# Performance work log

Hardware: AMD Instinct MI355X
Metric: run time of the kernel (lower is better)

The kernel has to match this reference:

```python
import jax, jax.numpy as jnp
import numpy as np

B, S, D, H, DH = 2, 2048, 1024, 16, 64
LN_EPS = 1e-5

def _layernorm(x, g, b):
    mu = jnp.mean(x, axis=-1, keepdims=True)
    var = jnp.mean(jnp.square(x - mu), axis=-1, keepdims=True)
    return (x - mu) * jax.lax.rsqrt(var + LN_EPS) * g + b

def setup_inputs() -> dict:
    key = jax.random.key(0)
    ks = jax.random.split(key, 12)
    s = 0.02
    return {
        'x': jax.random.normal(ks[0], (B, S, D), jnp.float32),
        'attention_mask': jnp.zeros((B, S), jnp.bool_),
        'Wq': jax.random.normal(ks[1], (H, D, DH), jnp.float32) * s,
        'bq': jnp.zeros((H, DH), jnp.float32),
        'Wk': jax.random.normal(ks[2], (H, D, DH), jnp.float32) * s,
        'bk': jnp.zeros((H, DH), jnp.float32),
        'Wv': jax.random.normal(ks[3], (H, D, DH), jnp.float32) * s,
        'bv': jnp.zeros((H, DH), jnp.float32),
        'ln_g': jnp.ones((D,), jnp.float32),
        'ln_b': jnp.zeros((D,), jnp.float32),
        'W1': jax.random.normal(ks[4], (D, 4 * D), jnp.float32) * s,
        'b1': jnp.zeros((4 * D,), jnp.float32),
        'W2': jax.random.normal(ks[5], (4 * D, D), jnp.float32) * s,
        'b2': jnp.zeros((D,), jnp.float32),
    }

def reference(x, attention_mask, Wq, bq, Wk, bk, Wv, bv, ln_g, ln_b, W1, b1, W2, b2):
    # NOTE: source has a typo bug ('attentoin_score'), so the attention_mask is
    # computed-then-discarded; softmax is applied to the UNMASKED scaled scores.
    dh = Wq.shape[-1]
    q = jnp.einsum('bsd,hde->bhse', x, Wq) + bq[:, None, :]  # [B,H,S,dh]
    k = jnp.einsum('bsd,hde->bhse', x, Wk) + bk[:, None, :]
    v = jnp.einsum('bsd,hde->bhse', x, Wv) + bv[:, None, :]
    scores = jnp.einsum('bhse,bhte->bhst', q, k) / jnp.sqrt(jnp.float32(dh))
    attn = jax.nn.softmax(scores, axis=-1)
    o = jnp.einsum('bhst,bhte->bhse', attn, v)  # [B,H,S,dh]
    b_, h_, s_, e_ = o.shape
    # concat heads along last dim == transpose then reshape
    mha = jnp.transpose(o, (0, 2, 1, 3)).reshape(b_, s_, h_ * e_)
    h1 = _layernorm(x + mha, ln_g, ln_b)
    ffn = jax.nn.relu(h1 @ W1 + b1) @ W2 + b2
    return _layernorm(h1 + ffn, ln_g, ln_b)
```

## Files before the change

kernel.cpp:

```cpp
#include <hip/hip_runtime.h>

#define DEVI __device__ __forceinline__

typedef __attribute__((ext_vector_type(8))) __bf16 bf16x8;
typedef __attribute__((ext_vector_type(4))) float f32x4;
typedef __attribute__((ext_vector_type(4))) unsigned short u16x4;
typedef __attribute__((ext_vector_type(8))) unsigned short u16x8;

static DEVI unsigned short f2bf(float f) {
  unsigned int i = __float_as_uint(f);
  i += 0x7fffu + ((i >> 16) & 1u);
  return (unsigned short)(i >> 16);
}

static DEVI unsigned short f2bfh(float f) {
  union { __bf16 h; unsigned short u; } c;
  c.h = (__bf16)f;
  return c.u;
}

static DEVI float bf2f(unsigned short u) {
  return __uint_as_float((unsigned int)u << 16);
}

static DEVI f32x4 mfma16x16x32(bf16x8 a, bf16x8 b, f32x4 c) {
  return __builtin_amdgcn_mfma_f32_16x16x32_bf16(a, b, c, 0, 0, 0);
}

static DEVI void async_ld16(const void* g, void* lds) {
  __builtin_amdgcn_global_load_lds(
      (const __attribute__((address_space(1))) void*)g,
      (__attribute__((address_space(3))) void*)lds, 16, 0, 0);
}

template <int BN, int OUT_MODE, bool RELU>
static DEVI void gemm_bt_core(const unsigned short* __restrict__ A, int lda,
                              const unsigned short* __restrict__ Bt, int ldb,
                              int K, int m0, int n0,
                              const float* __restrict__ bias,
                              void* __restrict__ Cp, int ldc,
                              const float* __restrict__ bq,
                              const float* __restrict__ bk,
                              const float* __restrict__ bv,
                              unsigned short* __restrict__ qo,
                              unsigned short* __restrict__ ko,
                              unsigned short* __restrict__ vo) {
  constexpr int MT = (BN == 128) ? 4 : 2;
  constexpr int NT = 4;
  __shared__ __align__(16) unsigned short As[128 * 32];
  __shared__ __align__(16) unsigned short Bs[BN * 32];

  const int tid = threadIdx.x;
  const int w = tid >> 6, l = tid & 63;
  const int lr = l & 15, lq = l >> 4;
  const int wm0 = (BN == 128) ? ((w >> 1) * 64) : (w * 32);
  const int wn0 = (BN == 128) ? ((w & 1) * 64) : 0;
  const int lrow = l >> 2;
  const int lcol = (l & 3) * 8;

  f32x4 acc[MT][NT];
#pragma unroll
  for (int i = 0; i < MT; ++i)
#pragma unroll
    for (int j = 0; j < NT; ++j) acc[i][j] = (f32x4){0.f, 0.f, 0.f, 0.f};

  for (int kb = 0; kb < K; kb += 32) {
#pragma unroll
    for (int p = 0; p < 2; ++p) {
      const int r0 = p * 64 + w * 16;
      async_ld16(A + (size_t)(m0 + r0 + lrow) * lda + kb + lcol, As + r0 * 32);
    }
#pragma unroll
    for (int p = 0; p < BN / 64; ++p) {
      const int r0 = p * 64 + w * 16;
      async_ld16(Bt + (size_t)(n0 + r0 + lrow) * ldb + kb + lcol, Bs + r0 * 32);
    }
    __syncthreads();

    bf16x8 af[MT], bfr[NT];
#pragma unroll
    for (int mt = 0; mt < MT; ++mt)
      af[mt] = *(const bf16x8*)(As + (wm0 + mt * 16 + lr) * 32 + lq * 8);
#pragma unroll
    for (int nt = 0; nt < NT; ++nt)
      bfr[nt] = *(const bf16x8*)(Bs + (wn0 + nt * 16 + lr) * 32 + lq * 8);
#pragma unroll
    for (int mt = 0; mt < MT; ++mt)
#pragma unroll
      for (int nt = 0; nt < NT; ++nt)
        acc[mt][nt] = mfma16x16x32(af[mt], bfr[nt], acc[mt][nt]);
    __syncthreads();
  }

#pragma unroll
  for (int mt = 0; mt < MT; ++mt) {
    const int grow = m0 + wm0 + mt * 16 + lq * 4;
#pragma unroll
    for (int nt = 0; nt < NT; ++nt) {
      const int gcol = n0 + wn0 + nt * 16 + lr;
      if (OUT_MODE == 2) {
        const int which = gcol >> 10;
        const int h = (gcol >> 6) & 15;
        const int e = gcol & 63;
        const float* bp = (which == 0) ? bq : (which == 1) ? bk : bv;
        const float bvv = bp[gcol & 1023];
        unsigned short* op = (which == 0) ? qo : (which == 1) ? ko : vo;
#pragma unroll
        for (int r = 0; r < 4; ++r) {
          const int row = grow + r;
          const int b_ = row >> 11, s_ = row & 2047;
          const size_t base = (size_t)((b_ << 4) + h) * 131072 + (size_t)s_ * 64;
          if (which == 1) {
            const int o = e >> 3;
            const int pos = (((o ^ (s_ & 7)) << 3) | (e & 7));
            op[base + pos] = f2bf((acc[mt][nt][r] + bvv) * 0.18033688011112f);
          } else {
            op[base + e] = f2bf(acc[mt][nt][r] + bvv);
          }
        }
      } else if (OUT_MODE == 3) {
#pragma unroll
        for (int r = 0; r < 4; ++r)
          ((unsigned short*)Cp)[(size_t)(grow + r) * ldc + gcol] =
              f2bf(acc[mt][nt][r]);
      } else {
        const float bvv = bias[gcol];
#pragma unroll
        for (int r = 0; r < 4; ++r) {
          float val = acc[mt][nt][r] + bvv;
          if (RELU) val = fmaxf(val, 0.f);
          if (OUT_MODE == 1)
            ((unsigned short*)Cp)[(size_t)(grow + r) * ldc + gcol] = f2bf(val);
          else
            ((float*)Cp)[(size_t)(grow + r) * ldc + gcol] = val;
        }
      }
    }
  }
}

__global__ __launch_bounds__(256) void k_gemm_qkv(
    const unsigned short* __restrict__ xb, const unsigned short* __restrict__ Wt,
    const float* __restrict__ bq, const float* __restrict__ bk,
    const float* __restrict__ bv, unsigned short* __restrict__ qo,
    unsigned short* __restrict__ ko, unsigned short* __restrict__ vo) {
  gemm_bt_core<128, 2, false>(xb, 1024, Wt, 1024, 1024, blockIdx.x * 128,
                              blockIdx.y * 128, nullptr, nullptr, 0, bq, bk, bv,
                              qo, ko, vo);
}

__global__ __launch_bounds__(256) void k_ffn1(
    const unsigned short* __restrict__ h1b, const unsigned short* __restrict__ W1t,
    const float* __restrict__ b1, unsigned short* __restrict__ f1) {
  gemm_bt_core<128, 1, true>(h1b, 1024, W1t, 1024, 1024, blockIdx.x * 128,
                             blockIdx.y * 128, b1, f1, 4096, nullptr, nullptr,
                             nullptr, nullptr, nullptr, nullptr);
}

__global__ __launch_bounds__(256) void k_ffn2(
    const unsigned short* __restrict__ f1, const unsigned short* __restrict__ W2t,
    unsigned short* __restrict__ pbase) {
  const int z = blockIdx.z;
  unsigned short* p = pbase + (size_t)z * 4194304;
  gemm_bt_core<128, 3, false>(f1 + z * 1024, 4096, W2t + z * 1024, 4096, 1024,
                              blockIdx.x * 128, blockIdx.y * 128, nullptr, p,
                              1024, nullptr, nullptr, nullptr, nullptr, nullptr,
                              nullptr);
}

__global__ __launch_bounds__(256) void k_cvt(const float* __restrict__ src,
                                             unsigned short* __restrict__ dst) {
  const size_t i = ((size_t)blockIdx.x * 256 + threadIdx.x) * 4;
  f32x4 v = *(const f32x4*)(src + i);
  u16x4 pk;
#pragma unroll
  for (int j = 0; j < 4; ++j) pk[j] = f2bf(v[j]);
  *(u16x4*)(dst + i) = pk;
}

static DEVI void tr64(const float* __restrict__ s, int sld,
                      unsigned short* __restrict__ d, int dld) {
  __shared__ float t[64][65];
  const int tr = threadIdx.x >> 4;
  const int tc4 = (threadIdx.x & 15) * 4;
#pragma unroll
  for (int i = 0; i < 4; ++i) {
    f32x4 v = *(const f32x4*)(s + (size_t)(i * 16 + tr) * sld + tc4);
#pragma unroll
    for (int j = 0; j < 4; ++j) t[i * 16 + tr][tc4 + j] = v[j];
  }
  __syncthreads();
#pragma unroll
  for (int i = 0; i < 4; ++i) {
    const int c = i * 16 + tr;
    u16x4 pk;
#pragma unroll
    for (int j = 0; j < 4; ++j) pk[j] = f2bf(t[tc4 + j][c]);
    *(u16x4*)(d + (size_t)c * dld + tc4) = pk;
  }
}

__global__ __launch_bounds__(256) void k_twall(
    const float* __restrict__ Wq, const float* __restrict__ Wk,
    const float* __restrict__ Wv, const float* __restrict__ W1,
    const float* __restrict__ W2, unsigned short* __restrict__ wqkvt,
    unsigned short* __restrict__ w1t, unsigned short* __restrict__ w2t) {
  const int bid = blockIdx.x;
  if (bid < 768) {
    const int bx = bid & 15, by = bid >> 4;
    const int which = by >> 4, h = by & 15;
    const float* W = (which == 0) ? Wq : (which == 1) ? Wk : Wv;
    const float* s = W + (size_t)h * 65536;
    unsigned short* d = wqkvt + (size_t)(which * 1024 + h * 64) * 1024;
    const int r0 = bx * 64;
    tr64(s + (size_t)r0 * 64, 64, d + r0, 1024);
  } else if (bid < 1792) {
    const int t = bid - 768;
    const int bx = t & 15, by = t >> 4;
    const int r0 = bx * 64, c0 = by * 64;
    tr64(W1 + (size_t)r0 * 4096 + c0, 4096, w1t + (size_t)c0 * 1024 + r0, 1024);
  } else {
    const int t = bid - 1792;
    const int bx = t & 63, by = t >> 6;
    const int r0 = bx * 64, c0 = by * 64;
    tr64(W2 + (size_t)r0 * 1024 + c0, 1024, w2t + (size_t)c0 * 4096 + r0, 4096);
  }
}

__global__ __launch_bounds__(256) void k_vprep(const unsigned short* __restrict__ vb,
                                               unsigned short* __restrict__ vp) {
  const int bh = blockIdx.y, t = blockIdx.x;
  __shared__ unsigned short tl[64][72];
  const int tid = threadIdx.x;
  const size_t base = (size_t)bh * 131072;
  const int kr = tid >> 3, oc = tid & 7;
#pragma unroll
  for (int p = 0; p < 2; ++p) {
    const int key = p * 32 + kr;
    *(u16x8*)&tl[key][oc * 8] =
        *(const u16x8*)(vb + base + (size_t)(t * 64 + key) * 64 + oc * 8);
  }
  __syncthreads();
#pragma unroll
  for (int p = 0; p < 2; ++p) {
    const int dh = p * 32 + kr;
    const int ok = oc ^ (dh & 7);
    u16x8 pk;
#pragma unroll
    for (int j = 0; j < 8; ++j) {
      const int kap = ok * 8 + j;
      const int key = (kap & 3) * 16 + (kap >> 2);
      pk[j] = tl[key][dh];
    }
    *(u16x8*)(vp + base + (size_t)dh * 2048 + t * 64 + oc * 8) = pk;
  }
}

__global__ __launch_bounds__(512) void k_attn(
    const unsigned short* __restrict__ q, const unsigned short* __restrict__ ks,
    const unsigned short* __restrict__ vp, float* __restrict__ mha) {
  const int bid = blockIdx.x;
  const int bh = (bid & 7) * 4 + ((bid >> 3) >> 4);
  const int qt = (bid >> 3) & 15;
  const int b = bh >> 4, h = bh & 15;
  const int tid = threadIdx.x;
  const int w = tid >> 6, l = tid & 63;
  const int lr = l & 15, lq = l >> 4, l7 = lr & 7;

  __shared__ __align__(16) unsigned short Ks[2][64 * 64];
  __shared__ __align__(16) unsigned short Vt[2][64 * 64];
  __shared__ __align__(16) unsigned short Ps[8][16][72];

  const size_t bho = (size_t)bh * 131072;
  const int q0 = qt * 128 + w * 16;

  bf16x8 qf0, qf1;
  {
    const unsigned short* qp = q + bho + (size_t)(q0 + lr) * 64 + lq * 8;
    qf0 = *(const bf16x8*)qp;
    qf1 = *(const bf16x8*)(qp + 32);
  }

  f32x4 l_acc[4];
  f32x4 o[4];
#pragma unroll
  for (int i = 0; i < 4; ++i) {
    l_acc[i] = (f32x4){0.f, 0.f, 0.f, 0.f};
    o[i] = (f32x4){0.f, 0.f, 0.f, 0.f};
  }

  const unsigned short* kg = ks + bho;
  const unsigned short* vg = vp + bho;
  const int srow = l >> 3, scol = (l & 7) * 8;
  const int r0 = w * 8;

  async_ld16(kg + (size_t)(r0 + srow) * 64 + scol, &Ks[0][r0 * 64]);
  async_ld16(vg + (size_t)(r0 + srow) * 2048 + scol, &Vt[0][r0 * 64]);
  __syncthreads();

  for (int kt = 0; kt < 32; ++kt) {
    const int cur = kt & 1, nxt = cur ^ 1;
    if (kt + 1 < 32) {
      const int k1 = (kt + 1) * 64;
      async_ld16(kg + (size_t)(k1 + r0 + srow) * 64 + scol, &Ks[nxt][r0 * 64]);
      async_ld16(vg + (size_t)(r0 + srow) * 2048 + k1 + scol, &Vt[nxt][r0 * 64]);
    }

    bf16x8 kf[4][2];
#pragma unroll
    for (int ct = 0; ct < 4; ++ct)
#pragma unroll
      for (int hh = 0; hh < 2; ++hh)
        kf[ct][hh] = *(const bf16x8*)&Ks[cur][(ct * 16 + lr) * 64 +
                                             (((hh << 2) | lq) ^ l7) * 8];
    f32x4 s[4];
#pragma unroll
    for (int ct = 0; ct < 4; ++ct) {
      f32x4 t = {0.f, 0.f, 0.f, 0.f};
      t = mfma16x16x32(qf0, kf[ct][0], t);
      t = mfma16x16x32(qf1, kf[ct][1], t);
      s[ct] = t;
    }

#pragma unroll
    for (int r = 0; r < 4; ++r) {
      f32x4 pe;
#pragma unroll
      for (int ct = 0; ct < 4; ++ct)
        pe[ct] = __builtin_amdgcn_exp2f(s[ct][r]);
      l_acc[r] += pe;
      u16x4 pk;
#pragma unroll
      for (int ct = 0; ct < 4; ++ct) pk[ct] = f2bfh(pe[ct]);
      *(u16x4*)&Ps[w][lq * 4 + r][lr * 4] = pk;
    }
    __asm__ volatile("" ::: "memory");

    bf16x8 vf[4][2];
#pragma unroll
    for (int dt = 0; dt < 4; ++dt)
#pragma unroll
      for (int hh = 0; hh < 2; ++hh)
        vf[dt][hh] = *(const bf16x8*)&Vt[cur][(dt * 16 + lr) * 64 +
                                             (((hh << 2) | lq) ^ l7) * 8];
    bf16x8 pf0 = *(const bf16x8*)&Ps[w][lr][lq * 8];
    bf16x8 pf1 = *(const bf16x8*)&Ps[w][lr][32 + lq * 8];
#pragma unroll
    for (int dt = 0; dt < 4; ++dt) {
      o[dt] = mfma16x16x32(pf0, vf[dt][0], o[dt]);
      o[dt] = mfma16x16x32(pf1, vf[dt][1], o[dt]);
    }
    __syncthreads();
  }

#pragma unroll
  for (int r = 0; r < 4; ++r) {
    f32x4 la = l_acc[r];
    float sd = la[0] + la[1] + la[2] + la[3];
    sd += __shfl_xor(sd, 1);
    sd += __shfl_xor(sd, 2);
    sd += __shfl_xor(sd, 4);
    sd += __shfl_xor(sd, 8);
    const float inv = 1.f / sd;
    float* op = mha + ((size_t)b * 2048 + q0 + lq * 4 + r) * 1024 + h * 64 + lr;
    op[0] = o[0][r] * inv;
    op[16] = o[1][r] * inv;
    op[32] = o[2][r] * inv;
    op[48] = o[3][r] * inv;
  }
}

__global__ __launch_bounds__(256) void k_add_ln(const float* __restrict__ a,
                                                const float* __restrict__ b,
                                                const float* __restrict__ g,
                                                const float* __restrict__ be,
                                                unsigned short* __restrict__ outb) {
  const int row = blockIdx.x;
  const int tid = threadIdx.x;
  const size_t base = (size_t)row * 1024 + tid * 4;
  f32x4 va = *(const f32x4*)(a + base);
  f32x4 vb = *(const f32x4*)(b + base);
  f32x4 xx;
  float s = 0.f, q = 0.f;
#pragma unroll
  for (int i = 0; i < 4; ++i) {
    xx[i] = va[i] + vb[i];
    s += xx[i];
    q += xx[i] * xx[i];
  }
#pragma unroll
  for (int off = 1; off < 64; off <<= 1) {
    s += __shfl_xor(s, off);
    q += __shfl_xor(q, off);
  }
  __shared__ float ss[4], qs[4];
  const int w = tid >> 6;
  if ((tid & 63) == 0) { ss[w] = s; qs[w] = q; }
  __syncthreads();
  s = ss[0] + ss[1] + ss[2] + ss[3];
  q = qs[0] + qs[1] + qs[2] + qs[3];
  const float mean = s * (1.f / 1024.f);
  const float var = q * (1.f / 1024.f) - mean * mean;
  const float rstd = rsqrtf(var + 1e-5f);
  f32x4 vg = *(const f32x4*)(g + tid * 4);
  f32x4 vbe = *(const f32x4*)(be + tid * 4);
  u16x4 pk;
#pragma unroll
  for (int i = 0; i < 4; ++i)
    pk[i] = f2bf((xx[i] - mean) * rstd * vg[i] + vbe[i]);
  *(u16x4*)(outb + base) = pk;
}

__global__ __launch_bounds__(256) void k_add_ln4(
    const unsigned short* __restrict__ h1b, const unsigned short* __restrict__ pb,
    const float* __restrict__ cb, const float* __restrict__ g,
    const float* __restrict__ be, float* __restrict__ out) {
  const int row = blockIdx.x;
  const int tid = threadIdx.x;
  const size_t base = (size_t)row * 1024 + tid * 4;
  u16x4 uh = *(const u16x4*)(h1b + base);
  u16x4 up[4];
#pragma unroll
  for (int z = 0; z < 4; ++z)
    up[z] = *(const u16x4*)(pb + base + (size_t)z * 4194304);
  f32x4 vcb = *(const f32x4*)(cb + tid * 4);
  f32x4 xx;
  float s = 0.f, q = 0.f;
#pragma unroll
  for (int i = 0; i < 4; ++i) {
    float v = bf2f(uh[i]) + vcb[i];
#pragma unroll
    for (int z = 0; z < 4; ++z) v += bf2f(up[z][i]);
    xx[i] = v;
    s += v;
    q += v * v;
  }
#pragma unroll
  for (int off = 1; off < 64; off <<= 1) {
    s += __shfl_xor(s, off);
    q += __shfl_xor(q, off);
  }
  __shared__ float ss[4], qs[4];
  const int w = tid >> 6;
  if ((tid & 63) == 0) { ss[w] = s; qs[w] = q; }
  __syncthreads();
  s = ss[0] + ss[1] + ss[2] + ss[3];
  q = qs[0] + qs[1] + qs[2] + qs[3];
  const float mean = s * (1.f / 1024.f);
  const float var = q * (1.f / 1024.f) - mean * mean;
  const float rstd = rsqrtf(var + 1e-5f);
  f32x4 vg = *(const f32x4*)(g + tid * 4);
  f32x4 vbe = *(const f32x4*)(be + tid * 4);
  f32x4 ov;
#pragma unroll
  for (int i = 0; i < 4; ++i) ov[i] = (xx[i] - mean) * rstd * vg[i] + vbe[i];
  *(f32x4*)(out + base) = ov;
}

extern "C" void kernel_launch(void* const* d_in, const int* in_sizes, int n_in,
                              void* d_out, int out_size, void* d_ws,
                              size_t ws_size, hipStream_t stream) {
  const float* x = (const float*)d_in[0];
  const float* Wq = (const float*)d_in[2];
  const float* bq = (const float*)d_in[3];
  const float* Wk = (const float*)d_in[4];
  const float* bk = (const float*)d_in[5];
  const float* Wv = (const float*)d_in[6];
  const float* bv = (const float*)d_in[7];
  const float* lg = (const float*)d_in[8];
  const float* lb = (const float*)d_in[9];
  const float* W1 = (const float*)d_in[10];
  const float* b1 = (const float*)d_in[11];
  const float* W2 = (const float*)d_in[12];
  const float* b2 = (const float*)d_in[13];

  char* ws = (char*)d_ws;
  const size_t MB = 1024 * 1024;
  unsigned short* qb = (unsigned short*)(ws + 0);
  unsigned short* kb = (unsigned short*)(ws + 8 * MB);
  unsigned short* vb = (unsigned short*)(ws + 16 * MB);
  unsigned short* vp = (unsigned short*)(ws + 24 * MB);
  unsigned short* f1 = (unsigned short*)(ws + 0);
  unsigned short* xb = (unsigned short*)(ws + 32 * MB);
  unsigned short* pb = (unsigned short*)(ws + 32 * MB);
  float* mha = (float*)(ws + 40 * MB);
  unsigned short* h1b = (unsigned short*)(ws + 64 * MB);
  unsigned short* wqkvt = (unsigned short*)(ws + 72 * MB);
  unsigned short* w1t = (unsigned short*)(ws + 78 * MB);
  unsigned short* w2t = (unsigned short*)(ws + 86 * MB);

  k_cvt<<<dim3(4096), 256, 0, stream>>>(x, xb);
  k_twall<<<dim3(2816), 256, 0, stream>>>(Wq, Wk, Wv, W1, W2, wqkvt, w1t, w2t);

  k_gemm_qkv<<<dim3(32, 24), 256, 0, stream>>>(xb, wqkvt, bq, bk, bv, qb, kb, vb);
  k_vprep<<<dim3(32, 32), 256, 0, stream>>>(vb, vp);
  k_attn<<<dim3(512), 512, 0, stream>>>(qb, kb, vp, mha);
  k_add_ln<<<dim3(4096), 256, 0, stream>>>(x, mha, lg, lb, h1b);
  k_ffn1<<<dim3(32, 32), 256, 0, stream>>>(h1b, w1t, b1, f1);
  k_ffn2<<<dim3(32, 8, 4), 256, 0, stream>>>(f1, w2t, pb);
  k_add_ln4<<<dim3(4096), 256, 0, stream>>>(h1b, pb, b2, lg, lb, (float*)d_out);
}
```

Baseline: 324.0 us.

## Fuse V permutation into QKV GEMM epilogue, merge prep kernels, store attention output bf16

The QKV GEMM epilogue now writes V straight into the swizzled, transposed layout that attention consumes, so the separate k_vprep kernel and its intermediate buffer are gone. The x-to-bf16 conversion is folded into the weight-transpose kernel as one k_prep launch. The attention output is stored as bf16 instead of fp32, which halves that write and the read in the add+layernorm kernel. The cost is scattered 2-byte stores for V in the epilogue and reduced precision on the attention output before the residual add.

```diff
diff --git a/kernel.cpp b/kernel.cpp
--- a/kernel.cpp
+++ b/kernel.cpp
@@ -104,18 +104,23 @@
         const int e = gcol & 63;
         const float* bp = (which == 0) ? bq : (which == 1) ? bk : bv;
         const float bvv = bp[gcol & 1023];
-        unsigned short* op = (which == 0) ? qo : (which == 1) ? ko : vo;
 #pragma unroll
         for (int r = 0; r < 4; ++r) {
           const int row = grow + r;
           const int b_ = row >> 11, s_ = row & 2047;
-          const size_t base = (size_t)((b_ << 4) + h) * 131072 + (size_t)s_ * 64;
-          if (which == 1) {
+          const size_t base = (size_t)((b_ << 4) + h) * 131072;
+          const float val = acc[mt][nt][r] + bvv;
+          if (which == 0) {
+            qo[base + (size_t)s_ * 64 + e] = f2bf(val);
+          } else if (which == 1) {
             const int o = e >> 3;
             const int pos = (((o ^ (s_ & 7)) << 3) | (e & 7));
-            op[base + pos] = f2bf((acc[mt][nt][r] + bvv) * 0.18033688011112f);
+            ko[base + (size_t)s_ * 64 + pos] = f2bf(val * 0.18033688011112f);
           } else {
-            op[base + e] = f2bf(acc[mt][nt][r] + bvv);
+            const int t = s_ >> 6, k64 = s_ & 63;
+            const int kap = (k64 & 15) * 4 + (k64 >> 4);
+            const int pos = (((kap >> 3) ^ (e & 7)) << 3) | (kap & 7);
+            vo[base + (size_t)e * 2048 + t * 64 + pos] = f2bf(val);
           }
         }
       } else if (OUT_MODE == 3) {
@@ -168,16 +173,6 @@
                               nullptr);
 }
 
-__global__ __launch_bounds__(256) void k_cvt(const float* __restrict__ src,
-                                             unsigned short* __restrict__ dst) {
-  const size_t i = ((size_t)blockIdx.x * 256 + threadIdx.x) * 4;
-  f32x4 v = *(const f32x4*)(src + i);
-  u16x4 pk;
-#pragma unroll
-  for (int j = 0; j < 4; ++j) pk[j] = f2bf(v[j]);
-  *(u16x4*)(dst + i) = pk;
-}
-
 static DEVI void tr64(const float* __restrict__ s, int sld,
                       unsigned short* __restrict__ d, int dld) {
   __shared__ float t[64][65];
@@ -200,65 +195,48 @@
   }
 }
 
-__global__ __launch_bounds__(256) void k_twall(
-    const float* __restrict__ Wq, const float* __restrict__ Wk,
-    const float* __restrict__ Wv, const float* __restrict__ W1,
-    const float* __restrict__ W2, unsigned short* __restrict__ wqkvt,
+__global__ __launch_bounds__(256) void k_prep(
+    const float* __restrict__ x, const float* __restrict__ Wq,
+    const float* __restrict__ Wk, const float* __restrict__ Wv,
+    const float* __restrict__ W1, const float* __restrict__ W2,
+    unsigned short* __restrict__ xb, unsigned short* __restrict__ wqkvt,
     unsigned short* __restrict__ w1t, unsigned short* __restrict__ w2t) {
   const int bid = blockIdx.x;
-  if (bid < 768) {
-    const int bx = bid & 15, by = bid >> 4;
+  if (bid < 1024) {
+    const size_t i0 = ((size_t)bid * 256 + threadIdx.x) * 16;
+#pragma unroll
+    for (int c = 0; c < 4; ++c) {
+      f32x4 v = *(const f32x4*)(x + i0 + c * 4);
+      u16x4 pk;
+#pragma unroll
+      for (int j = 0; j < 4; ++j) pk[j] = f2bf(v[j]);
+      *(u16x4*)(xb + i0 + c * 4) = pk;
+    }
+  } else if (bid < 1792) {
+    const int t = bid - 1024;
+    const int bx = t & 15, by = t >> 4;
     const int which = by >> 4, h = by & 15;
     const float* W = (which == 0) ? Wq : (which == 1) ? Wk : Wv;
     const float* s = W + (size_t)h * 65536;
     unsigned short* d = wqkvt + (size_t)(which * 1024 + h * 64) * 1024;
     const int r0 = bx * 64;
     tr64(s + (size_t)r0 * 64, 64, d + r0, 1024);
-  } else if (bid < 1792) {
-    const int t = bid - 768;
+  } else if (bid < 2816) {
+    const int t = bid - 1792;
     const int bx = t & 15, by = t >> 4;
     const int r0 = bx * 64, c0 = by * 64;
     tr64(W1 + (size_t)r0 * 4096 + c0, 4096, w1t + (size_t)c0 * 1024 + r0, 1024);
   } else {
-    const int t = bid - 1792;
+    const int t = bid - 2816;
     const int bx = t & 63, by = t >> 6;
     const int r0 = bx * 64, c0 = by * 64;
     tr64(W2 + (size_t)r0 * 1024 + c0, 1024, w2t + (size_t)c0 * 4096 + r0, 4096);
   }
 }
 
-__global__ __launch_bounds__(256) void k_vprep(const unsigned short* __restrict__ vb,
-                                               unsigned short* __restrict__ vp) {
-  const int bh = blockIdx.y, t = blockIdx.x;
-  __shared__ unsigned short tl[64][72];
-  const int tid = threadIdx.x;
-  const size_t base = (size_t)bh * 131072;
-  const int kr = tid >> 3, oc = tid & 7;
-#pragma unroll
-  for (int p = 0; p < 2; ++p) {
-    const int key = p * 32 + kr;
-    *(u16x8*)&tl[key][oc * 8] =
-        *(const u16x8*)(vb + base + (size_t)(t * 64 + key) * 64 + oc * 8);
-  }
-  __syncthreads();
-#pragma unroll
-  for (int p = 0; p < 2; ++p) {
-    const int dh = p * 32 + kr;
-    const int ok = oc ^ (dh & 7);
-    u16x8 pk;
-#pragma unroll
-    for (int j = 0; j < 8; ++j) {
-      const int kap = ok * 8 + j;
-      const int key = (kap & 3) * 16 + (kap >> 2);
-      pk[j] = tl[key][dh];
-    }
-    *(u16x8*)(vp + base + (size_t)dh * 2048 + t * 64 + oc * 8) = pk;
-  }
-}
-
 __global__ __launch_bounds__(512) void k_attn(
     const unsigned short* __restrict__ q, const unsigned short* __restrict__ ks,
-    const unsigned short* __restrict__ vp, float* __restrict__ mha) {
+    const unsigned short* __restrict__ vp, unsigned short* __restrict__ mha) {
   const int bid = blockIdx.x;
   const int bh = (bid & 7) * 4 + ((bid >> 3) >> 4);
   const int qt = (bid >> 3) & 15;
@@ -362,16 +340,17 @@
     sd += __shfl_xor(sd, 4);
     sd += __shfl_xor(sd, 8);
     const float inv = 1.f / sd;
-    float* op = mha + ((size_t)b * 2048 + q0 + lq * 4 + r) * 1024 + h * 64 + lr;
-    op[0] = o[0][r] * inv;
-    op[16] = o[1][r] * inv;
-    op[32] = o[2][r] * inv;
-    op[48] = o[3][r] * inv;
+    unsigned short* op =
+        mha + ((size_t)b * 2048 + q0 + lq * 4 + r) * 1024 + h * 64 + lr;
+    op[0] = f2bfh(o[0][r] * inv);
+    op[16] = f2bfh(o[1][r] * inv);
+    op[32] = f2bfh(o[2][r] * inv);
+    op[48] = f2bfh(o[3][r] * inv);
   }
 }
 
 __global__ __launch_bounds__(256) void k_add_ln(const float* __restrict__ a,
-                                                const float* __restrict__ b,
+                                                const unsigned short* __restrict__ b,
                                                 const float* __restrict__ g,
                                                 const float* __restrict__ be,
                                                 unsigned short* __restrict__ outb) {
@@ -379,12 +358,12 @@
   const int tid = threadIdx.x;
   const size_t base = (size_t)row * 1024 + tid * 4;
   f32x4 va = *(const f32x4*)(a + base);
-  f32x4 vb = *(const f32x4*)(b + base);
+  u16x4 ub = *(const u16x4*)(b + base);
   f32x4 xx;
   float s = 0.f, q = 0.f;
 #pragma unroll
   for (int i = 0; i < 4; ++i) {
-    xx[i] = va[i] + vb[i];
+    xx[i] = va[i] + bf2f(ub[i]);
     s += xx[i];
     q += xx[i] * xx[i];
   }
@@ -478,22 +457,19 @@
   const size_t MB = 1024 * 1024;
   unsigned short* qb = (unsigned short*)(ws + 0);
   unsigned short* kb = (unsigned short*)(ws + 8 * MB);
-  unsigned short* vb = (unsigned short*)(ws + 16 * MB);
-  unsigned short* vp = (unsigned short*)(ws + 24 * MB);
+  unsigned short* vp = (unsigned short*)(ws + 16 * MB);
   unsigned short* f1 = (unsigned short*)(ws + 0);
   unsigned short* xb = (unsigned short*)(ws + 32 * MB);
   unsigned short* pb = (unsigned short*)(ws + 32 * MB);
-  float* mha = (float*)(ws + 40 * MB);
+  unsigned short* mha = (unsigned short*)(ws + 40 * MB);
   unsigned short* h1b = (unsigned short*)(ws + 64 * MB);
   unsigned short* wqkvt = (unsigned short*)(ws + 72 * MB);
   unsigned short* w1t = (unsigned short*)(ws + 78 * MB);
   unsigned short* w2t = (unsigned short*)(ws + 86 * MB);
 
-  k_cvt<<<dim3(4096), 256, 0, stream>>>(x, xb);
-  k_twall<<<dim3(2816), 256, 0, stream>>>(Wq, Wk, Wv, W1, W2, wqkvt, w1t, w2t);
-
-  k_gemm_qkv<<<dim3(32, 24), 256, 0, stream>>>(xb, wqkvt, bq, bk, bv, qb, kb, vb);
-  k_vprep<<<dim3(32, 32), 256, 0, stream>>>(vb, vp);
+  k_prep<<<dim3(3840), 256, 0, stream>>>(x, Wq, Wk, Wv, W1, W2, xb, wqkvt, w1t,
+                                         w2t);
+  k_gemm_qkv<<<dim3(32, 24), 256, 0, stream>>>(xb, wqkvt, bq, bk, bv, qb, kb, vp);
   k_attn<<<dim3(512), 512, 0, stream>>>(qb, kb, vp, mha);
   k_add_ln<<<dim3(4096), 256, 0, stream>>>(x, mha, lg, lb, h1b);
   k_ffn1<<<dim3(32, 32), 256, 0, stream>>>(h1b, w1t, b1, f1);
```

New measurement: 322.9 us. About the same (-0.4%).
